# Optimization experiments

Hardware: AMD Instinct MI355X
Metric: run time of the kernel (lower is better)

The kernel has to match this reference:

```python
import jax, jax.numpy as jnp
import numpy as np
from jax import lax


def _xavier(key, shape):
    fan_out, fan_in = shape
    lim = float(np.sqrt(6.0 / (fan_in + fan_out)))
    return jax.random.uniform(key, shape, jnp.float32, -lim, lim)


def setup_inputs() -> dict:
    V, E, H, F, B = 32000, 512, 256, 256, 64
    key = jax.random.key(0)
    ks = jax.random.split(key, 16)
    emb = _xavier(ks[0], (V, E)).at[0].set(0.0)  # padding_idx=0 zeroed
    return {
        'enc_feat': jax.random.normal(ks[1], (B, F), jnp.float32),
        'emb': emb,
        'Wh': _xavier(ks[2], (H, F)), 'bh': jnp.zeros((H,), jnp.float32),
        'Wc': _xavier(ks[3], (H, F)), 'bc': jnp.zeros((H,), jnp.float32),
        'Wih0': _xavier(ks[4], (4 * H, E)), 'Whh0': _xavier(ks[5], (4 * H, H)),
        'bih0': jnp.zeros((4 * H,), jnp.float32), 'bhh0': jnp.zeros((4 * H,), jnp.float32),
        'Wih1': _xavier(ks[6], (4 * H, H)), 'Whh1': _xavier(ks[7], (4 * H, H)),
        'bih1': jnp.zeros((4 * H,), jnp.float32), 'bhh1': jnp.zeros((4 * H,), jnp.float32),
        'Wout': _xavier(ks[8], (V, H)), 'bout': jnp.zeros((V,), jnp.float32),
        'sos_id': 1, 'eos_id': 2, 'max_len': 48,
    }


def _lstm_cell(x, h, c, Wih, Whh, bih, bhh):
    # PyTorch gate order: i, f, g, o
    g = x @ Wih.T + h @ Whh.T + (bih + bhh)
    i, f, gg, o = jnp.split(g, 4, axis=-1)
    c_new = jax.nn.sigmoid(f) * c + jax.nn.sigmoid(i) * jnp.tanh(gg)
    h_new = jax.nn.sigmoid(o) * jnp.tanh(c_new)
    return h_new, c_new


def reference(enc_feat, emb, Wh, bh, Wc, bc, Wih0, Whh0, bih0, bhh0,
              Wih1, Whh1, bih1, bhh1, Wout, bout, sos_id, eos_id, max_len):
    B = enc_feat.shape[0]
    h_init = enc_feat @ Wh.T + bh  # [B, H], repeated over num_layers
    c_init = enc_feat @ Wc.T + bc
    tok0 = jnp.full((B,), sos_id, jnp.int32)
    carry0 = (tok0, h_init, c_init, h_init, c_init,
              jnp.zeros((B,), bool), jnp.array(False))

    def step(carry, _):
        tok, h0, c0, h1, c1, done, all_done = carry
        x = emb[tok]                                   # [B, E]
        h0, c0 = _lstm_cell(x, h0, c0, Wih0, Whh0, bih0, bhh0)
        h1, c1 = _lstm_cell(h0, h1, c1, Wih1, Whh1, bih1, bhh1)
        logits = h1 @ Wout.T + bout                    # [B, V]
        nt = jnp.argmax(logits, axis=-1).astype(jnp.int32)  # greedy decode
        out = jnp.where(all_done, 0, nt)               # torch pads with 0 after break
        done = done | (out == eos_id)
        all_done = all_done | jnp.all(done)
        return (out, h0, c0, h1, c1, done, all_done), out

    _, toks = lax.scan(step, carry0, None, length=max_len)  # [max_len, B]
    return toks.T.astype(jnp.int64)  # [B, max_len]
```

## Files before the change

### kernel.cpp

```cpp
#include <hip/hip_runtime.h>
#include <math.h>

#define TSTEPS 48
#define NCELL 32
#define ND 224
#define NBLK (NCELL + ND)

#define OFF_W0T   0
#define OFF_W1T   524288
#define OFF_WH0T  786432
#define OFF_WH1T  1048576
#define OFF_BS0   1310720
#define OFF_BS1   1311744
#define OFF_HINIT 1312768
#define OFF_CINIT 1329152
#define OFF_H0BUF 1345536
#define OFF_H1BUF 1361920
#define OFF_FLOAT_END 1378304

#define FSTR 32
#define FL_H0F   0
#define FL_H1C   1024
#define FL_H1ALL 2048
#define FL_DFLAG 3072
#define FL_DMIR  10240
#define FL_TOK   11264
#define NFLAGU32 12288

typedef float f4v __attribute__((ext_vector_type(4)));

__device__ __forceinline__ unsigned ld_cohu(const unsigned* p) {
  return __hip_atomic_load((unsigned*)p, __ATOMIC_RELAXED, __HIP_MEMORY_SCOPE_AGENT);
}
__device__ __forceinline__ void st_cohu(unsigned* p, unsigned v) {
  __hip_atomic_store(p, v, __ATOMIC_RELAXED, __HIP_MEMORY_SCOPE_AGENT);
}
__device__ __forceinline__ unsigned long long ld_coh64(const unsigned long long* p) {
  return __hip_atomic_load((unsigned long long*)p, __ATOMIC_RELAXED, __HIP_MEMORY_SCOPE_AGENT);
}
__device__ __forceinline__ void st_coh64(unsigned long long* p, unsigned long long v) {
  __hip_atomic_store(p, v, __ATOMIC_RELAXED, __HIP_MEMORY_SCOPE_AGENT);
}
__device__ __forceinline__ float4 ldg_coh_f4(const float4* p) {
  f4v r;
  asm volatile("global_load_dwordx4 %0, %1, off sc0 sc1\n\ts_waitcnt vmcnt(0)"
               : "=v"(r) : "v"(p) : "memory");
  return make_float4(r.x, r.y, r.z, r.w);
}
__device__ __forceinline__ void ldg_coh_f4x4(const float4* p0, const float4* p1,
                                             const float4* p2, const float4* p3,
                                             float4& a, float4& b, float4& c, float4& d) {
  f4v ra, rb, rc, rd;
  asm volatile(
      "global_load_dwordx4 %0, %4, off sc0 sc1\n\t"
      "global_load_dwordx4 %1, %5, off sc0 sc1\n\t"
      "global_load_dwordx4 %2, %6, off sc0 sc1\n\t"
      "global_load_dwordx4 %3, %7, off sc0 sc1\n\t"
      "s_waitcnt vmcnt(0)"
      : "=&v"(ra), "=&v"(rb), "=&v"(rc), "=&v"(rd)
      : "v"(p0), "v"(p1), "v"(p2), "v"(p3) : "memory");
  a = make_float4(ra.x, ra.y, ra.z, ra.w);
  b = make_float4(rb.x, rb.y, rb.z, rb.w);
  c = make_float4(rc.x, rc.y, rc.z, rc.w);
  d = make_float4(rd.x, rd.y, rd.z, rd.w);
}
__device__ __forceinline__ void stg_coh_f4(float4* p, float4 v) {
  f4v t = {v.x, v.y, v.z, v.w};
  asm volatile("global_store_dwordx4 %0, %1, off sc0 sc1" :: "v"(p), "v"(t) : "memory");
}
__device__ __forceinline__ void drain_vm() {
  asm volatile("s_waitcnt vmcnt(0)" ::: "memory");
}
__device__ __forceinline__ float4 ldnt_f4(const float4* p) {
  f4v v = __builtin_nontemporal_load((const f4v*)p);
  return make_float4(v.x, v.y, v.z, v.w);
}
__device__ __forceinline__ float sigf(float x) { return 1.0f / (1.0f + expf(-x)); }
__device__ __forceinline__ unsigned long long u64max(unsigned long long a, unsigned long long b) {
  return a > b ? a : b;
}
__device__ __forceinline__ unsigned long long wmax64(unsigned long long k) {
#pragma unroll
  for (int off = 1; off < 64; off <<= 1) {
    unsigned long long o = __shfl_xor(k, off, 64);
    k = u64max(k, o);
  }
  return k;
}
__device__ __forceinline__ unsigned long long packkey(float lg, int v) {
  unsigned u = __float_as_uint(lg);
  u = (u & 0x80000000u) ? ~u : (u | 0x80000000u);
  return ((unsigned long long)u << 32) | (unsigned)(~(unsigned)v);
}
__device__ __forceinline__ float4 f4add(float4 a, float4 b) {
  return make_float4(a.x + b.x, a.y + b.y, a.z + b.z, a.w + b.w);
}

__global__ void lstm_init_kernel(const float* enc, const float* Wh, const float* bh,
                                 const float* Wc, const float* bc,
                                 const float* bih0, const float* bhh0,
                                 const float* bih1, const float* bhh1,
                                 float* ws, unsigned long long* key2, unsigned* flags) {
  const int tid = threadIdx.x, blk = blockIdx.x;
  if (blk < 64) {
    __shared__ float el[256];
    el[tid] = enc[blk * 256 + tid];
    __syncthreads();
    const float4* el4 = (const float4*)el;
    const float4* wh4 = (const float4*)(Wh + tid * 256);
    const float4* wc4 = (const float4*)(Wc + tid * 256);
    float ah = bh[tid], ac = bc[tid];
#pragma unroll 4
    for (int f = 0; f < 64; ++f) {
      float4 x = el4[f], a = wh4[f], b = wc4[f];
      ah = fmaf(a.x, x.x, fmaf(a.y, x.y, fmaf(a.z, x.z, fmaf(a.w, x.w, ah))));
      ac = fmaf(b.x, x.x, fmaf(b.y, x.y, fmaf(b.z, x.z, fmaf(b.w, x.w, ac))));
    }
    ws[OFF_HINIT + blk * 256 + tid] = ah;
    ws[OFF_CINIT + blk * 256 + tid] = ac;
  } else if (blk == 64) {
    for (int g = tid; g < 1024; g += 256) {
      int hh = g >> 9, gc = g & 511;
      int row = (gc >> 7) * 256 + hh * 128 + (gc & 127);
      ws[OFF_BS0 + g] = bih0[row] + bhh0[row];
      ws[OFF_BS1 + g] = bih1[row] + bhh1[row];
    }
  } else {
    const int base = (blk - 65) * 256 + tid;
    for (int i = base; i < 64 * 256; i += 15 * 256) key2[i] = 0ull;
    for (int i = base; i < NFLAGU32; i += 15 * 256) flags[i] = 0u;
  }
}

__global__ void lstm_relayout_kernel(const float* Wih0, const float* Whh0,
                                     const float* Wih1, const float* Whh1, float* ws) {
  const int gid = blockIdx.x * 256 + threadIdx.x;
  const int gstr = 256 * 256;
  const float* srcs[4] = {Wih0, Wih1, Whh0, Whh1};
  const int dsts[4] = {OFF_W0T, OFF_W1T, OFF_WH0T, OFF_WH1T};
  const int k4tot[4] = {128, 64, 64, 64};
  for (int s = 0; s < 4; ++s) {
    const int n = 2 * k4tot[s] * 512;
    float4* dst = (float4*)(ws + dsts[s]);
    const float4* src = (const float4*)srcs[s];
    for (int e = gid; e < n; e += gstr) {
      int hh = e / (k4tot[s] * 512);
      int r = e - hh * k4tot[s] * 512;
      int k4 = r / 512, gc = r - k4 * 512;
      int row = (gc >> 7) * 256 + hh * 128 + (gc & 127);
      dst[e] = src[(size_t)row * k4tot[s] + k4];
    }
  }
}

struct CellSm {
  float x[4 * 512];
  float4 part[1024];
  float4 r0res[512];
  float4 r1res[512];
  float h0[4 * 256];
  float h1[4 * 256];
  float c0[4 * 128];
  float c1[4 * 128];
  int tok[4];
  unsigned fm[32];
  unsigned long long fred[16];
  int done4;
  int alldone;
};
struct DSm {
  float w[16 * 144 * 4];
  float h[64 * 68];
  unsigned long long kr[128];
  unsigned long long epi[16 * 64];
};
union Smem { CellSm c; DSm d; };

template <int K4H>
__device__ __forceinline__ void gemv_half(const float4* __restrict__ W,
                                          const float* __restrict__ xl, int xstride,
                                          float4* __restrict__ part, int tid) {
  const int kh = tid >> 9;
  float a0 = 0.f, a1 = 0.f, a2 = 0.f, a3 = 0.f;
  const float4* wp = W + (size_t)(kh * K4H) * 512 + (tid & 511);
  const float* x0 = xl + kh * K4H * 4;
#pragma unroll 8
  for (int i = 0; i < K4H; ++i) {
    float4 w = wp[(size_t)i * 512];
    float4 xa = *(const float4*)(x0 + i * 4);
    float4 xb = *(const float4*)(x0 + xstride + i * 4);
    float4 xc = *(const float4*)(x0 + 2 * xstride + i * 4);
    float4 xd = *(const float4*)(x0 + 3 * xstride + i * 4);
    a0 = fmaf(w.x, xa.x, fmaf(w.y, xa.y, fmaf(w.z, xa.z, fmaf(w.w, xa.w, a0))));
    a1 = fmaf(w.x, xb.x, fmaf(w.y, xb.y, fmaf(w.z, xb.z, fmaf(w.w, xb.w, a1))));
    a2 = fmaf(w.x, xc.x, fmaf(w.y, xc.y, fmaf(w.z, xc.z, fmaf(w.w, xc.w, a2))));
    a3 = fmaf(w.x, xd.x, fmaf(w.y, xd.y, fmaf(w.z, xd.z, fmaf(w.w, xd.w, a3))));
  }
  part[tid] = make_float4(a0, a1, a2, a3);
}

__device__ __forceinline__ void cellfold(const float4* part, const float4* rres,
                                         const float* bs, float* cst, float* hst,
                                         int hh, int tid) {
  if (tid < 512) {
    int jj = tid & 127, b = tid >> 7;
    float g[4];
#pragma unroll
    for (int q = 0; q < 4; ++q) {
      int gc = q * 128 + jj;
      g[q] = ((const float*)&part[gc])[b] + ((const float*)&part[512 + gc])[b] +
             ((const float*)&rres[gc])[b] + bs[gc];
    }
    float c = cst[b * 128 + jj];
    float cn = sigf(g[1]) * c + sigf(g[0]) * tanhf(g[2]);
    float hn = sigf(g[3]) * tanhf(cn);
    cst[b * 128 + jj] = cn;
    hst[b * 256 + hh * 128 + jj] = hn;
  }
}

__global__ __launch_bounds__(1024, 4) void lstm_decode_kernel(
    const float* __restrict__ emb, const float* __restrict__ Wout,
    const float* __restrict__ bout, const int* __restrict__ sosp,
    const int* __restrict__ eosp, float* __restrict__ ws,
    unsigned long long* __restrict__ key2, unsigned* __restrict__ flags,
    int* __restrict__ out) {
  const int tid = threadIdx.x;
  const int blk = blockIdx.x;
  __shared__ Smem sm;
  const int eos = *eosp;
  const int sos = *sosp;
  float4* h0b4 = (float4*)(ws + OFF_H0BUF);
  float4* h1b4 = (float4*)(ws + OFF_H1BUF);

  if (blk < NCELL) {
    const int bg = blk >> 1, hh = blk & 1, ph = 1 - hh;
    const float4* W0 = (const float4*)(ws + OFF_W0T) + (size_t)hh * 128 * 512;
    const float4* W1 = (const float4*)(ws + OFF_W1T) + (size_t)hh * 64 * 512;
    const float4* WH0 = (const float4*)(ws + OFF_WH0T) + (size_t)hh * 64 * 512;
    const float4* WH1 = (const float4*)(ws + OFF_WH1T) + (size_t)hh * 64 * 512;
    const float* bs0 = ws + OFF_BS0 + hh * 512;
    const float* bs1 = ws + OFF_BS1 + hh * 512;

    {
      int b = tid >> 8, k = tid & 255;
      float hv = ws[OFF_HINIT + (bg * 4 + b) * 256 + k];
      sm.c.h0[b * 256 + k] = hv;
      sm.c.h1[b * 256 + k] = hv;
    }
    if (tid < 512) {
      int b = tid >> 7, jj = tid & 127;
      float cv = ws[OFF_CINIT + (bg * 4 + b) * 256 + hh * 128 + jj];
      sm.c.c0[b * 128 + jj] = cv;
      sm.c.c1[b * 128 + jj] = cv;
    }
    if (tid < 4) sm.c.tok[tid] = sos;
    if (tid == 0) { sm.c.done4 = 0; sm.c.alldone = 0; }
    __syncthreads();
    gemv_half<32>(WH0, sm.c.h0, 256, sm.c.part, tid);
    __syncthreads();
    if (tid < 512) sm.c.r0res[tid] = f4add(sm.c.part[tid], sm.c.part[512 + tid]);
    __syncthreads();
    gemv_half<32>(WH1, sm.c.h1, 256, sm.c.part, tid);
    __syncthreads();
    if (tid < 512) sm.c.r1res[tid] = f4add(sm.c.part[tid], sm.c.part[512 + tid]);
    __syncthreads();

    for (int t = 0; t < TSTEPS; ++t) {
      const unsigned T = (unsigned)(t + 1);
      if (tid < 512) {
        int b = tid >> 7, j = tid & 127;
        ((float4*)sm.c.x)[b * 128 + j] = ((const float4*)emb)[(size_t)sm.c.tok[b] * 128 + j];
      }
      __syncthreads();
      gemv_half<64>(W0, sm.c.x, 512, sm.c.part, tid);
      __syncthreads();
      cellfold(sm.c.part, sm.c.r0res, bs0, sm.c.c0, sm.c.h0, hh, tid);
      __syncthreads();
      if (tid < 128) {
        int b = tid >> 5, j = tid & 31;
        float4 v = *(float4*)&sm.c.h0[b * 256 + hh * 128 + j * 4];
        stg_coh_f4(h0b4 + (bg * 4 + b) * 64 + hh * 32 + j, v);
      }
      drain_vm();
      __syncthreads();
      if (tid == 0) {
        st_cohu(flags + FL_H0F + blk * FSTR, T);
        while (ld_cohu(flags + FL_H0F + (blk ^ 1) * FSTR) < T) __builtin_amdgcn_s_sleep(1);
      }
      __syncthreads();
      if (tid < 128) {
        int b = tid >> 5, j = tid & 31;
        float4 v = ldg_coh_f4(h0b4 + (bg * 4 + b) * 64 + ph * 32 + j);
        *(float4*)&sm.c.h0[b * 256 + ph * 128 + j * 4] = v;
      }
      __syncthreads();
      gemv_half<32>(W1, sm.c.h0, 256, sm.c.part, tid);
      __syncthreads();
      cellfold(sm.c.part, sm.c.r1res, bs1, sm.c.c1, sm.c.h1, hh, tid);
      __syncthreads();
      if (tid < 128) {
        int b = tid >> 5, j = tid & 31;
        float4 v = *(float4*)&sm.c.h1[b * 256 + hh * 128 + j * 4];
        stg_coh_f4(h1b4 + (bg * 4 + b) * 64 + hh * 32 + j, v);
      }
      drain_vm();
      __syncthreads();
      if (tid == 0) st_cohu(flags + FL_H1C + blk * FSTR, T);
      if (tid < 64) {
        unsigned v = T;
        for (;;) {
          if (tid < 32) v = ld_cohu(flags + FL_H1C + tid * FSTR);
          if (__all((int)(v >= T))) break;
          __builtin_amdgcn_s_sleep(1);
        }
      }
      __syncthreads();
      if (tid == 0) st_cohu(flags + FL_H1ALL + blk * FSTR, T);
      if (tid < 128) {
        int b = tid >> 5, j = tid & 31;
        float4 v = ldg_coh_f4(h1b4 + (bg * 4 + b) * 64 + ph * 32 + j);
        *(float4*)&sm.c.h1[b * 256 + ph * 128 + j * 4] = v;
      }
      __syncthreads();
      if (t > 0) {
        if (tid < 64) {
          unsigned tgt = (unsigned)t << 8;
          unsigned got = tgt;
          for (;;) {
            if (tid < 32) got = ld_cohu(flags + FL_TOK + tid * FSTR);
            if (__all((int)(got >= tgt))) break;
            __builtin_amdgcn_s_sleep(2);
          }
          if (tid < 32) sm.c.fm[tid] = got & 0xFFu;
        }
        __syncthreads();
        if (tid < 64) {
          int ok = 1;
          if (tid < 32) ok = (sm.c.fm[tid] == 0xFu);
          int all = __all(ok);
          if (tid == 0) sm.c.alldone = all;
        }
        __syncthreads();
      }
      gemv_half<32>(WH0, sm.c.h0, 256, sm.c.part, tid);
      __syncthreads();
      if (tid < 512) sm.c.r0res[tid] = f4add(sm.c.part[tid], sm.c.part[512 + tid]);
      __syncthreads();
      gemv_half<32>(WH1, sm.c.h1, 256, sm.c.part, tid);
      __syncthreads();
      if (tid < 512) sm.c.r1res[tid] = f4add(sm.c.part[tid], sm.c.part[512 + tid]);
      __syncthreads();
      if (tid < 64) {
        unsigned v = T;
        for (;;) {
          if (tid < 7) v = ld_cohu(flags + FL_DFLAG + (blk * 7 + tid) * FSTR);
          if (__all((int)(v >= T))) break;
          __builtin_amdgcn_s_sleep(4);
        }
      }
      __syncthreads();
      if (tid == 0) st_cohu(flags + FL_DMIR + blk * FSTR, T);
      if (tid < 64) {
        unsigned v = T;
        for (;;) {
          if (tid < 32) v = ld_cohu(flags + FL_DMIR + tid * FSTR);
          if (__all((int)(v >= T))) break;
          __builtin_amdgcn_s_sleep(2);
        }
      }
      __syncthreads();
      {
        int bb = tid >> 8, i = tid & 255;
        unsigned long long k = ld_coh64(key2 + (size_t)(bg * 4 + bb) * 256 + i);
        k = wmax64(k);
        if ((tid & 63) == 0) sm.c.fred[tid >> 6] = k;
      }
      __syncthreads();
      if (tid < 4) {
        int bb = tid;
        unsigned long long m = u64max(u64max(sm.c.fred[bb * 4], sm.c.fred[bb * 4 + 1]),
                                      u64max(sm.c.fred[bb * 4 + 2], sm.c.fred[bb * 4 + 3]));
        int v = (int)(~(unsigned)m);
        int outv = sm.c.alldone ? 0 : v;
        out[(bg * 4 + bb) * TSTEPS + t] = outv;
        int nd = ((sm.c.done4 >> bb) & 1) | (outv == eos ? 1 : 0);
        sm.c.tok[bb] = outv;
        sm.c.fm[bb] = (unsigned)nd;
      }
      __syncthreads();
      if (tid == 0) {
        int mask = (int)(sm.c.fm[0] | (sm.c.fm[1] << 1) | (sm.c.fm[2] << 2) | (sm.c.fm[3] << 3));
        sm.c.done4 = mask;
        if (t < TSTEPS - 1)
          st_cohu(flags + FL_TOK + blk * FSTR, ((unsigned)(t + 1) << 8) | (unsigned)mask);
      }
      __syncthreads();
    }
  } else {
    const int d = blk - NCELL;
    const int r0 = (d * 32000) / ND, r1 = ((d + 1) * 32000) / ND;
    const int rows = r1 - r0, nep = rows - 128;
    const int bg = tid >> 7, v = tid & 127;
    const int erow = tid >> 6, eb = tid & 63;
    const float4* Wout4 = (const float4*)Wout;
    const int nq = 144 * 16;

    for (int t = 0; t < TSTEPS; ++t) {
      const unsigned T = (unsigned)(t + 1);
      float4 wpre[3];
#pragma unroll
      for (int p = 0; p < 3; ++p) {
        int e = tid + p * 1024;
        if (e < nq) {
          int j = e / 144, r = e - j * 144;
          int rc = r0 + r; if (rc > 31999) rc = 31999;
          wpre[p] = ldnt_f4(Wout4 + (size_t)rc * 64 + j);
        } else wpre[p] = make_float4(0.f, 0.f, 0.f, 0.f);
      }
      if (tid == 0) {
        while (ld_cohu(flags + FL_H1ALL + (d & 31) * FSTR) < T) __builtin_amdgcn_s_sleep(4);
      }
      __syncthreads();
      float4 hpre[4];
      {
        int b = tid >> 4, j = tid & 15;
        const float4* hp = (const float4*)h1b4 + (size_t)b * 64 + j;
        ldg_coh_f4x4(hp, hp + 16, hp + 32, hp + 48, hpre[0], hpre[1], hpre[2], hpre[3]);
      }
      float acc[8];
#pragma unroll
      for (int i = 0; i < 8; ++i) acc[i] = 0.f;
      float eacc = 0.f;

      for (int kc = 0; kc < 4; ++kc) {
        __syncthreads();
#pragma unroll
        for (int p = 0; p < 3; ++p) {
          int e = tid + p * 1024;
          if (e < nq) {
            int j = e / 144, r = e - j * 144;
            *(float4*)&sm.d.w[(j * 144 + r) * 4] = wpre[p];
          }
        }
        {
          int b = tid >> 4, j = tid & 15;
          *(float4*)&sm.d.h[b * 68 + j * 4] = hpre[kc];
        }
        __syncthreads();
        if (kc < 3) {
#pragma unroll
          for (int p = 0; p < 3; ++p) {
            int e = tid + p * 1024;
            if (e < nq) {
              int j = e / 144, r = e - j * 144;
              int rc = r0 + r; if (rc > 31999) rc = 31999;
              wpre[p] = ldnt_f4(Wout4 + (size_t)rc * 64 + (kc + 1) * 16 + j);
            }
          }
        }
#pragma unroll 4
        for (int k4 = 0; k4 < 16; ++k4) {
          float4 w4 = *(const float4*)&sm.d.w[(k4 * 144 + v) * 4];
#pragma unroll
          for (int bi = 0; bi < 8; ++bi) {
            float4 h4 = *(const float4*)&sm.d.h[(bg * 8 + bi) * 68 + k4 * 4];
            acc[bi] = fmaf(w4.x, h4.x, fmaf(w4.y, h4.y, fmaf(w4.z, h4.z, fmaf(w4.w, h4.w, acc[bi]))));
          }
        }
        if (erow < nep) {
#pragma unroll 4
          for (int k4 = 0; k4 < 16; ++k4) {
            float4 w4 = *(const float4*)&sm.d.w[(k4 * 144 + 128 + erow) * 4];
            float4 h4 = *(const float4*)&sm.d.h[eb * 68 + k4 * 4];
            eacc = fmaf(w4.x, h4.x, fmaf(w4.y, h4.y, fmaf(w4.z, h4.z, fmaf(w4.w, h4.w, eacc))));
          }
        }
      }
      {
        float bb_ = bout[r0 + v];
#pragma unroll
        for (int bi = 0; bi < 8; ++bi) {
          unsigned long long k = packkey(acc[bi] + bb_, r0 + v);
          k = wmax64(k);
          if ((tid & 63) == 0) sm.d.kr[(bg * 8 + bi) * 2 + (v >> 6)] = k;
        }
      }
      if (erow < nep) {
        sm.d.epi[erow * 64 + eb] = packkey(eacc + bout[r0 + 128 + erow], r0 + 128 + erow);
      } else {
        sm.d.epi[erow * 64 + eb] = 0ull;
      }
      __syncthreads();
      if (tid < 64) {
        unsigned long long m = u64max(sm.d.kr[tid * 2], sm.d.kr[tid * 2 + 1]);
#pragma unroll
        for (int er = 0; er < 15; ++er) m = u64max(m, sm.d.epi[er * 64 + tid]);
        st_coh64(key2 + (size_t)tid * 256 + d, m);
      }
      drain_vm();
      __syncthreads();
      if (tid == 0) st_cohu(flags + FL_DFLAG + d * FSTR, T);
    }
  }
}

extern "C" void kernel_launch(void* const* d_in, const int* in_sizes, int n_in,
                              void* d_out, int out_size, void* d_ws, size_t ws_size,
                              hipStream_t stream) {
  const float* enc  = (const float*)d_in[0];
  const float* emb  = (const float*)d_in[1];
  const float* Wh   = (const float*)d_in[2];
  const float* bh   = (const float*)d_in[3];
  const float* Wc   = (const float*)d_in[4];
  const float* bc   = (const float*)d_in[5];
  const float* Wih0 = (const float*)d_in[6];
  const float* Whh0 = (const float*)d_in[7];
  const float* bih0 = (const float*)d_in[8];
  const float* bhh0 = (const float*)d_in[9];
  const float* Wih1 = (const float*)d_in[10];
  const float* Whh1 = (const float*)d_in[11];
  const float* bih1 = (const float*)d_in[12];
  const float* bhh1 = (const float*)d_in[13];
  const float* Wout = (const float*)d_in[14];
  const float* bout = (const float*)d_in[15];
  const int* sosp   = (const int*)d_in[16];
  const int* eosp   = (const int*)d_in[17];

  float* ws = (float*)d_ws;
  char* base = (char*)d_ws + (size_t)OFF_FLOAT_END * 4;
  unsigned long long* key2 = (unsigned long long*)base;
  unsigned* flags          = (unsigned*)(base + 131072);
  int* out = (int*)d_out;

  lstm_init_kernel<<<80, 256, 0, stream>>>(enc, Wh, bh, Wc, bc, bih0, bhh0,
                                           bih1, bhh1, ws, key2, flags);
  lstm_relayout_kernel<<<256, 256, 0, stream>>>(Wih0, Whh0, Wih1, Whh1, ws);
  lstm_decode_kernel<<<NBLK, 1024, 0, stream>>>(emb, Wout, bout, sosp, eosp,
                                                ws, key2, flags, out);
}
```

Measured before the change: 3.215 ms.

## Restructure vocab projection blocks to per-wave row ownership with direct weight loads

The vocab-projection blocks no longer stage Wout chunks through shared memory in four k-chunks with double-buffered prefetch. Each wavefront now owns 9 consecutive vocab rows, and each lane handles one batch element. The wave reads its weight rows straight from global or cache with wave-uniform addresses, and the full h vector is held in LDS in a skewed layout that avoids bank conflicts. This removes the staging barriers and the two-path main/epilogue split and reduces each block's argmax to one per-wave key. The cost is that weights are no longer loaded nontemporally, and the per-row loads are broadcast scalar-like reads that rely on cache hits rather than coalesced vector traffic.

New measurement: 4.154 ms. 1.29x slower.

```diff
diff --git a/kernel.cpp b/kernel.cpp
--- a/kernel.cpp
+++ b/kernel.cpp
@@ -70,10 +70,6 @@
 }
 __device__ __forceinline__ void drain_vm() {
   asm volatile("s_waitcnt vmcnt(0)" ::: "memory");
-}
-__device__ __forceinline__ float4 ldnt_f4(const float4* p) {
-  f4v v = __builtin_nontemporal_load((const f4v*)p);
-  return make_float4(v.x, v.y, v.z, v.w);
 }
 __device__ __forceinline__ float sigf(float x) { return 1.0f / (1.0f + expf(-x)); }
 __device__ __forceinline__ unsigned long long u64max(unsigned long long a, unsigned long long b) {
@@ -169,10 +165,7 @@
   int alldone;
 };
 struct DSm {
-  float w[16 * 144 * 4];
-  float h[64 * 68];
-  unsigned long long kr[128];
-  unsigned long long epi[16 * 64];
+  float4 hs[64 * 64];
 };
 union Smem { CellSm c; DSm d; };
 
@@ -400,102 +393,67 @@
   } else {
     const int d = blk - NCELL;
     const int r0 = (d * 32000) / ND, r1 = ((d + 1) * 32000) / ND;
-    const int rows = r1 - r0, nep = rows - 128;
-    const int bg = tid >> 7, v = tid & 127;
-    const int erow = tid >> 6, eb = tid & 63;
-    const float4* Wout4 = (const float4*)Wout;
-    const int nq = 144 * 16;
+    const int l = tid & 63;
+    const int wv_ = __builtin_amdgcn_readfirstlane(tid >> 6);
+    const int rowbase = r0 + wv_ * 9;
+
+    int rcl[9];
+    const float* wrp[9];
+    float bb[9];
+#pragma unroll
+    for (int r = 0; r < 9; ++r) {
+      int rr = rowbase + r;
+      rcl[r] = (rr < r1) ? rr : (r1 - 1);
+      wrp[r] = Wout + (size_t)rcl[r] * 256;
+      bb[r] = bout[rcl[r]];
+    }
+    unsigned long long* kx = (unsigned long long*)sm.d.hs;
 
     for (int t = 0; t < TSTEPS; ++t) {
       const unsigned T = (unsigned)(t + 1);
-      float4 wpre[3];
-#pragma unroll
-      for (int p = 0; p < 3; ++p) {
-        int e = tid + p * 1024;
-        if (e < nq) {
-          int j = e / 144, r = e - j * 144;
-          int rc = r0 + r; if (rc > 31999) rc = 31999;
-          wpre[p] = ldnt_f4(Wout4 + (size_t)rc * 64 + j);
-        } else wpre[p] = make_float4(0.f, 0.f, 0.f, 0.f);
-      }
       if (tid == 0) {
         while (ld_cohu(flags + FL_H1ALL + (d & 31) * FSTR) < T) __builtin_amdgcn_s_sleep(4);
       }
       __syncthreads();
-      float4 hpre[4];
       {
         int b = tid >> 4, j = tid & 15;
         const float4* hp = (const float4*)h1b4 + (size_t)b * 64 + j;
-        ldg_coh_f4x4(hp, hp + 16, hp + 32, hp + 48, hpre[0], hpre[1], hpre[2], hpre[3]);
-      }
-      float acc[8];
-#pragma unroll
-      for (int i = 0; i < 8; ++i) acc[i] = 0.f;
-      float eacc = 0.f;
-
-      for (int kc = 0; kc < 4; ++kc) {
-        __syncthreads();
-#pragma unroll
-        for (int p = 0; p < 3; ++p) {
-          int e = tid + p * 1024;
-          if (e < nq) {
-            int j = e / 144, r = e - j * 144;
-            *(float4*)&sm.d.w[(j * 144 + r) * 4] = wpre[p];
-          }
-        }
-        {
-          int b = tid >> 4, j = tid & 15;
-          *(float4*)&sm.d.h[b * 68 + j * 4] = hpre[kc];
-        }
-        __syncthreads();
-        if (kc < 3) {
-#pragma unroll
-          for (int p = 0; p < 3; ++p) {
-            int e = tid + p * 1024;
-            if (e < nq) {
-              int j = e / 144, r = e - j * 144;
-              int rc = r0 + r; if (rc > 31999) rc = 31999;
-              wpre[p] = ldnt_f4(Wout4 + (size_t)rc * 64 + (kc + 1) * 16 + j);
-            }
-          }
-        }
-#pragma unroll 4
-        for (int k4 = 0; k4 < 16; ++k4) {
-          float4 w4 = *(const float4*)&sm.d.w[(k4 * 144 + v) * 4];
-#pragma unroll
-          for (int bi = 0; bi < 8; ++bi) {
-            float4 h4 = *(const float4*)&sm.d.h[(bg * 8 + bi) * 68 + k4 * 4];
-            acc[bi] = fmaf(w4.x, h4.x, fmaf(w4.y, h4.y, fmaf(w4.z, h4.z, fmaf(w4.w, h4.w, acc[bi]))));
-          }
-        }
-        if (erow < nep) {
-#pragma unroll 4
-          for (int k4 = 0; k4 < 16; ++k4) {
-            float4 w4 = *(const float4*)&sm.d.w[(k4 * 144 + 128 + erow) * 4];
-            float4 h4 = *(const float4*)&sm.d.h[eb * 68 + k4 * 4];
-            eacc = fmaf(w4.x, h4.x, fmaf(w4.y, h4.y, fmaf(w4.z, h4.z, fmaf(w4.w, h4.w, eacc))));
-          }
-        }
-      }
-      {
-        float bb_ = bout[r0 + v];
-#pragma unroll
-        for (int bi = 0; bi < 8; ++bi) {
-          unsigned long long k = packkey(acc[bi] + bb_, r0 + v);
-          k = wmax64(k);
-          if ((tid & 63) == 0) sm.d.kr[(bg * 8 + bi) * 2 + (v >> 6)] = k;
-        }
-      }
-      if (erow < nep) {
-        sm.d.epi[erow * 64 + eb] = packkey(eacc + bout[r0 + 128 + erow], r0 + 128 + erow);
-      } else {
-        sm.d.epi[erow * 64 + eb] = 0ull;
-      }
+        float4 h0_, h1_, h2_, h3_;
+        ldg_coh_f4x4(hp, hp + 16, hp + 32, hp + 48, h0_, h1_, h2_, h3_);
+        float4 hv[4] = {h0_, h1_, h2_, h3_};
+#pragma unroll
+        for (int p = 0; p < 4; ++p) {
+          int k4 = j + 16 * p;
+          sm.d.hs[(k4 << 6) + ((b + k4) & 63)] = hv[p];
+        }
+      }
+      __syncthreads();
+
+      float acc[9];
+#pragma unroll
+      for (int r = 0; r < 9; ++r) acc[r] = 0.f;
+
+#pragma unroll 2
+      for (int k4 = 0; k4 < 64; ++k4) {
+        float4 h4 = sm.d.hs[(k4 << 6) + ((l + k4) & 63)];
+#pragma unroll
+        for (int r = 0; r < 9; ++r) {
+          float4 w4 = *(const float4*)(wrp[r] + (k4 << 2));
+          acc[r] = fmaf(w4.x, h4.x, fmaf(w4.y, h4.y, fmaf(w4.z, h4.z, fmaf(w4.w, h4.w, acc[r]))));
+        }
+      }
+
+      unsigned long long kb = packkey(acc[0] + bb[0], rcl[0]);
+#pragma unroll
+      for (int r = 1; r < 9; ++r) kb = u64max(kb, packkey(acc[r] + bb[r], rcl[r]));
+
+      __syncthreads();
+      kx[wv_ * 64 + l] = kb;
       __syncthreads();
       if (tid < 64) {
-        unsigned long long m = u64max(sm.d.kr[tid * 2], sm.d.kr[tid * 2 + 1]);
-#pragma unroll
-        for (int er = 0; er < 15; ++er) m = u64max(m, sm.d.epi[er * 64 + tid]);
+        unsigned long long m = kx[tid];
+#pragma unroll
+        for (int w2 = 1; w2 < 16; ++w2) m = u64max(m, kx[w2 * 64 + tid]);
         st_coh64(key2 + (size_t)tid * 256 + d, m);
       }
       drain_vm();
```

## Rebalance LSTM gemv to two columns per thread and remap vocab-block thread work

Applied to the files above, without the earlier changes.

The cell-block gemv now runs on 512 threads, each computing two output columns so every activation load from LDS is reused across two weight rows, leaving the other 512 threads idle. The vocab projection blocks are remapped so each thread owns one row in each of three row groups (including the extra 'epilogue' rows) over 4 batch entries. This folds the separate epilogue loop and its LDS buffer into the main loop and reduces the final argmax to a single wave reduction per batch. The gemv change halves active lanes, which trades LDS traffic for less latency hiding on weight loads.

New measurement: 5.077 ms. +57.9%, slower.

```diff
diff --git a/kernel.cpp b/kernel.cpp
--- a/kernel.cpp
+++ b/kernel.cpp
@@ -172,31 +172,41 @@
   float w[16 * 144 * 4];
   float h[64 * 68];
   unsigned long long kr[128];
-  unsigned long long epi[16 * 64];
 };
 union Smem { CellSm c; DSm d; };
 
 template <int K4H>
-__device__ __forceinline__ void gemv_half(const float4* __restrict__ W,
-                                          const float* __restrict__ xl, int xstride,
-                                          float4* __restrict__ part, int tid) {
-  const int kh = tid >> 9;
-  float a0 = 0.f, a1 = 0.f, a2 = 0.f, a3 = 0.f;
-  const float4* wp = W + (size_t)(kh * K4H) * 512 + (tid & 511);
-  const float* x0 = xl + kh * K4H * 4;
+__device__ __forceinline__ void gemv_two(const float4* __restrict__ W,
+                                         const float* __restrict__ xl, int xstride,
+                                         float4* __restrict__ part, int tid) {
+  if (tid < 512) {
+    const int kh = tid >> 8;
+    const int p = tid & 255;
+    float a0 = 0.f, a1 = 0.f, a2 = 0.f, a3 = 0.f;
+    float b0 = 0.f, b1 = 0.f, b2 = 0.f, b3 = 0.f;
+    const float4* wp0 = W + (size_t)(kh * K4H) * 512 + p;
+    const float4* wp1 = wp0 + 256;
+    const float* x0 = xl + kh * K4H * 4;
 #pragma unroll 8
-  for (int i = 0; i < K4H; ++i) {
-    float4 w = wp[(size_t)i * 512];
-    float4 xa = *(const float4*)(x0 + i * 4);
-    float4 xb = *(const float4*)(x0 + xstride + i * 4);
-    float4 xc = *(const float4*)(x0 + 2 * xstride + i * 4);
-    float4 xd = *(const float4*)(x0 + 3 * xstride + i * 4);
-    a0 = fmaf(w.x, xa.x, fmaf(w.y, xa.y, fmaf(w.z, xa.z, fmaf(w.w, xa.w, a0))));
-    a1 = fmaf(w.x, xb.x, fmaf(w.y, xb.y, fmaf(w.z, xb.z, fmaf(w.w, xb.w, a1))));
-    a2 = fmaf(w.x, xc.x, fmaf(w.y, xc.y, fmaf(w.z, xc.z, fmaf(w.w, xc.w, a2))));
-    a3 = fmaf(w.x, xd.x, fmaf(w.y, xd.y, fmaf(w.z, xd.z, fmaf(w.w, xd.w, a3))));
+    for (int i = 0; i < K4H; ++i) {
+      float4 w0 = wp0[(size_t)i * 512];
+      float4 w1 = wp1[(size_t)i * 512];
+      float4 xa = *(const float4*)(x0 + i * 4);
+      float4 xb = *(const float4*)(x0 + xstride + i * 4);
+      float4 xc = *(const float4*)(x0 + 2 * xstride + i * 4);
+      float4 xd = *(const float4*)(x0 + 3 * xstride + i * 4);
+      a0 = fmaf(w0.x, xa.x, fmaf(w0.y, xa.y, fmaf(w0.z, xa.z, fmaf(w0.w, xa.w, a0))));
+      a1 = fmaf(w0.x, xb.x, fmaf(w0.y, xb.y, fmaf(w0.z, xb.z, fmaf(w0.w, xb.w, a1))));
+      a2 = fmaf(w0.x, xc.x, fmaf(w0.y, xc.y, fmaf(w0.z, xc.z, fmaf(w0.w, xc.w, a2))));
+      a3 = fmaf(w0.x, xd.x, fmaf(w0.y, xd.y, fmaf(w0.z, xd.z, fmaf(w0.w, xd.w, a3))));
+      b0 = fmaf(w1.x, xa.x, fmaf(w1.y, xa.y, fmaf(w1.z, xa.z, fmaf(w1.w, xa.w, b0))));
+      b1 = fmaf(w1.x, xb.x, fmaf(w1.y, xb.y, fmaf(w1.z, xb.z, fmaf(w1.w, xb.w, b1))));
+      b2 = fmaf(w1.x, xc.x, fmaf(w1.y, xc.y, fmaf(w1.z, xc.z, fmaf(w1.w, xc.w, b2))));
+      b3 = fmaf(w1.x, xd.x, fmaf(w1.y, xd.y, fmaf(w1.z, xd.z, fmaf(w1.w, xd.w, b3))));
+    }
+    part[kh * 512 + p] = make_float4(a0, a1, a2, a3);
+    part[kh * 512 + p + 256] = make_float4(b0, b1, b2, b3);
   }
-  part[tid] = make_float4(a0, a1, a2, a3);
 }
 
 __device__ __forceinline__ void cellfold(const float4* part, const float4* rres,
@@ -257,11 +267,11 @@
     if (tid < 4) sm.c.tok[tid] = sos;
     if (tid == 0) { sm.c.done4 = 0; sm.c.alldone = 0; }
     __syncthreads();
-    gemv_half<32>(WH0, sm.c.h0, 256, sm.c.part, tid);
+    gemv_two<32>(WH0, sm.c.h0, 256, sm.c.part, tid);
     __syncthreads();
     if (tid < 512) sm.c.r0res[tid] = f4add(sm.c.part[tid], sm.c.part[512 + tid]);
     __syncthreads();
-    gemv_half<32>(WH1, sm.c.h1, 256, sm.c.part, tid);
+    gemv_two<32>(WH1, sm.c.h1, 256, sm.c.part, tid);
     __syncthreads();
     if (tid < 512) sm.c.r1res[tid] = f4add(sm.c.part[tid], sm.c.part[512 + tid]);
     __syncthreads();
@@ -273,7 +283,7 @@
         ((float4*)sm.c.x)[b * 128 + j] = ((const float4*)emb)[(size_t)sm.c.tok[b] * 128 + j];
       }
       __syncthreads();
-      gemv_half<64>(W0, sm.c.x, 512, sm.c.part, tid);
+      gemv_two<64>(W0, sm.c.x, 512, sm.c.part, tid);
       __syncthreads();
       cellfold(sm.c.part, sm.c.r0res, bs0, sm.c.c0, sm.c.h0, hh, tid);
       __syncthreads();
@@ -295,7 +305,7 @@
         *(float4*)&sm.c.h0[b * 256 + ph * 128 + j * 4] = v;
       }
       __syncthreads();
-      gemv_half<32>(W1, sm.c.h0, 256, sm.c.part, tid);
+      gemv_two<32>(W1, sm.c.h0, 256, sm.c.part, tid);
       __syncthreads();
       cellfold(sm.c.part, sm.c.r1res, bs1, sm.c.c1, sm.c.h1, hh, tid);
       __syncthreads();
@@ -343,11 +353,11 @@
         }
         __syncthreads();
       }
-      gemv_half<32>(WH0, sm.c.h0, 256, sm.c.part, tid);
+      gemv_two<32>(WH0, sm.c.h0, 256, sm.c.part, tid);
       __syncthreads();
       if (tid < 512) sm.c.r0res[tid] = f4add(sm.c.part[tid], sm.c.part[512 + tid]);
       __syncthreads();
-      gemv_half<32>(WH1, sm.c.h1, 256, sm.c.part, tid);
+      gemv_two<32>(WH1, sm.c.h1, 256, sm.c.part, tid);
       __syncthreads();
       if (tid < 512) sm.c.r1res[tid] = f4add(sm.c.part[tid], sm.c.part[512 + tid]);
       __syncthreads();
@@ -401,10 +411,13 @@
     const int d = blk - NCELL;
     const int r0 = (d * 32000) / ND, r1 = ((d + 1) * 32000) / ND;
     const int rows = r1 - r0, nep = rows - 128;
-    const int bg = tid >> 7, v = tid & 127;
-    const int erow = tid >> 6, eb = tid & 63;
+    const int v = tid & 63, bq = tid >> 6;
     const float4* Wout4 = (const float4*)Wout;
     const int nq = 144 * 16;
+
+    const float bbA = bout[r0 + v];
+    const float bbB = bout[r0 + 64 + v];
+    const float bbE = (v < nep) ? bout[r0 + 128 + v] : 0.f;
 
     for (int t = 0; t < TSTEPS; ++t) {
       const unsigned T = (unsigned)(t + 1);
@@ -428,10 +441,9 @@
         const float4* hp = (const float4*)h1b4 + (size_t)b * 64 + j;
         ldg_coh_f4x4(hp, hp + 16, hp + 32, hp + 48, hpre[0], hpre[1], hpre[2], hpre[3]);
       }
-      float acc[8];
-#pragma unroll
-      for (int i = 0; i < 8; ++i) acc[i] = 0.f;
-      float eacc = 0.f;
+      float accA[4], accB[4], eacc[4];
+#pragma unroll
+      for (int i = 0; i < 4; ++i) { accA[i] = 0.f; accB[i] = 0.f; eacc[i] = 0.f; }
 
       for (int kc = 0; kc < 4; ++kc) {
         __syncthreads();
@@ -461,43 +473,29 @@
         }
 #pragma unroll 4
         for (int k4 = 0; k4 < 16; ++k4) {
-          float4 w4 = *(const float4*)&sm.d.w[(k4 * 144 + v) * 4];
-#pragma unroll
-          for (int bi = 0; bi < 8; ++bi) {
-            float4 h4 = *(const float4*)&sm.d.h[(bg * 8 + bi) * 68 + k4 * 4];
-            acc[bi] = fmaf(w4.x, h4.x, fmaf(w4.y, h4.y, fmaf(w4.z, h4.z, fmaf(w4.w, h4.w, acc[bi]))));
+          float4 wA = *(const float4*)&sm.d.w[(k4 * 144 + v) * 4];
+          float4 wB = *(const float4*)&sm.d.w[(k4 * 144 + 64 + v) * 4];
+          float4 wE = make_float4(0.f, 0.f, 0.f, 0.f);
+          if (v < nep) wE = *(const float4*)&sm.d.w[(k4 * 144 + 128 + v) * 4];
+#pragma unroll
+          for (int bi = 0; bi < 4; ++bi) {
+            float4 h4 = *(const float4*)&sm.d.h[(bq * 4 + bi) * 68 + k4 * 4];
+            accA[bi] = fmaf(wA.x, h4.x, fmaf(wA.y, h4.y, fmaf(wA.z, h4.z, fmaf(wA.w, h4.w, accA[bi]))));
+            accB[bi] = fmaf(wB.x, h4.x, fmaf(wB.y, h4.y, fmaf(wB.z, h4.z, fmaf(wB.w, h4.w, accB[bi]))));
+            eacc[bi] = fmaf(wE.x, h4.x, fmaf(wE.y, h4.y, fmaf(wE.z, h4.z, fmaf(wE.w, h4.w, eacc[bi]))));
           }
         }
-        if (erow < nep) {
-#pragma unroll 4
-          for (int k4 = 0; k4 < 16; ++k4) {
-            float4 w4 = *(const float4*)&sm.d.w[(k4 * 144 + 128 + erow) * 4];
-            float4 h4 = *(const float4*)&sm.d.h[eb * 68 + k4 * 4];
-            eacc = fmaf(w4.x, h4.x, fmaf(w4.y, h4.y, fmaf(w4.z, h4.z, fmaf(w4.w, h4.w, eacc))));
-          }
-        }
-      }
-      {
-        float bb_ = bout[r0 + v];
-#pragma unroll
-        for (int bi = 0; bi < 8; ++bi) {
-          unsigned long long k = packkey(acc[bi] + bb_, r0 + v);
-          k = wmax64(k);
-          if ((tid & 63) == 0) sm.d.kr[(bg * 8 + bi) * 2 + (v >> 6)] = k;
-        }
-      }
-      if (erow < nep) {
-        sm.d.epi[erow * 64 + eb] = packkey(eacc + bout[r0 + 128 + erow], r0 + 128 + erow);
-      } else {
-        sm.d.epi[erow * 64 + eb] = 0ull;
-      }
-      __syncthreads();
-      if (tid < 64) {
-        unsigned long long m = u64max(sm.d.kr[tid * 2], sm.d.kr[tid * 2 + 1]);
-#pragma unroll
-        for (int er = 0; er < 15; ++er) m = u64max(m, sm.d.epi[er * 64 + tid]);
-        st_coh64(key2 + (size_t)tid * 256 + d, m);
-      }
+      }
+#pragma unroll
+      for (int bi = 0; bi < 4; ++bi) {
+        unsigned long long k = packkey(accA[bi] + bbA, r0 + v);
+        k = u64max(k, packkey(accB[bi] + bbB, r0 + 64 + v));
+        if (v < nep) k = u64max(k, packkey(eacc[bi] + bbE, r0 + 128 + v));
+        k = wmax64(k);
+        if (v == 0) sm.d.kr[bq * 4 + bi] = k;
+      }
+      __syncthreads();
+      if (tid < 64) st_coh64(key2 + (size_t)tid * 256 + d, sm.d.kr[tid]);
       drain_vm();
       __syncthreads();
       if (tid == 0) st_cohu(flags + FL_DFLAG + d * FSTR, T);
```
